# Kernel optimization log

Hardware: AMD Instinct MI355X
Metric: run time of the kernel (lower is better)

Reference implementation:

```python
import jax, jax.numpy as jnp
import numpy as np

INPUT_DIM = 362
HIDDEN = 256
STYLE_NUM = 60
OUTFIT_NUM = 49710
BATCH = 16384


def setup_inputs() -> dict:
    key = jax.random.key(0)
    ks = jax.random.split(key, 12)
    f32 = jnp.float32
    return {
        "i_feature": jax.random.normal(ks[0], (BATCH, INPUT_DIM), f32),
        "j_feature": jax.random.normal(ks[1], (BATCH, INPUT_DIM), f32),
        "k_feature": jax.random.normal(ks[2], (BATCH, INPUT_DIM), f32),
        # top_emb / bottom_emb Linear params (stored transposed: x @ W + b)
        "W_top": jax.random.normal(ks[3], (INPUT_DIM, HIDDEN), f32) * 0.05,
        "b_top": jnp.zeros((HIDDEN,), f32),
        "W_bot": jax.random.normal(ks[4], (INPUT_DIM, HIDDEN), f32) * 0.05,
        "b_bot": jnp.zeros((HIDDEN,), f32),
        # NMF factors (forward relu_'s them in place; we relu on use)
        "P_nmf": jax.random.normal(ks[5], (2 * INPUT_DIM, STYLE_NUM), f32),
        "N_nmf": jax.random.normal(ks[6], (2 * INPUT_DIM, STYLE_NUM), f32),
        "H1_nmf": jax.random.normal(ks[7], (STYLE_NUM, OUTFIT_NUM), f32),
        "H2_nmf": jax.random.normal(ks[8], (STYLE_NUM, OUTFIT_NUM), f32),
        "matirx_pos": jax.random.uniform(ks[9], (2 * INPUT_DIM, OUTFIT_NUM), f32),
        "matirx_neg": jax.random.uniform(ks[10], (2 * INPUT_DIM, OUTFIT_NUM), f32),
    }


def _emb(x, W, b):
    # nn.Sequential(Linear, Sigmoid)
    return jax.nn.sigmoid(x @ W + b)


def _style_score(i_f, j_f, styles, W_top, b_top, W_bot, b_bot):
    # Vectorized version of the per-sample loop:
    # squared-distance argmin codebook lookup + gather + rowwise dot.
    outfit = jnp.concatenate([i_f, j_f], axis=1)  # [B, 2D]
    # mean over feature dim of (x - s)^2; constant 1/(2D) scale does not change argmin
    d2 = (jnp.sum(outfit * outfit, axis=1, keepdims=True)
          - 2.0 * (outfit @ styles)
          + jnp.sum(styles * styles, axis=0, keepdims=True))  # [B, S]
    idx = jnp.argmin(d2, axis=1)                               # [B]
    sel = styles.T[idx]                                        # [B, 2D] gather
    top, bot = sel[:, :INPUT_DIM], sel[:, INPUT_DIM:]
    # diag(matmul) == rowwise dot
    return jnp.sum(_emb(top, W_top, b_top) * _emb(bot, W_bot, b_bot), axis=1)  # [B]


def reference(i_feature, j_feature, k_feature, W_top, b_top, W_bot, b_bot,
              P_nmf, N_nmf, H1_nmf, H2_nmf, matirx_pos, matirx_neg):
    Ti = _emb(i_feature, W_top, b_top)   # [B, H]
    Bj = _emb(j_feature, W_bot, b_bot)   # [B, H]
    Bk = _emb(k_feature, W_bot, b_bot)   # [B, H]
    # torch.diag(matmul(Ti, Bj.T)) == rowwise dot (avoids [B,B] intermediate)
    ij_score = jnp.sum(Ti * Bj, axis=1)  # [B]
    ik_score = jnp.sum(Ti * Bk, axis=1)  # [B]

    # forward does relu_ on .data before use
    P = jnp.maximum(P_nmf, 0.0)
    N = jnp.maximum(N_nmf, 0.0)
    H1 = jnp.maximum(H1_nmf, 0.0)
    H2 = jnp.maximum(H2_nmf, 0.0)

    style_ij = _style_score(i_feature, j_feature, P, W_top, b_top, W_bot, b_bot)
    style_ik = _style_score(i_feature, k_feature, N, W_top, b_top, W_bot, b_bot)

    # -mean(log(sigmoid(d))) computed stably
    loss1 = -jnp.mean(jax.nn.log_sigmoid(ij_score - ik_score))
    loss2 = -jnp.mean(jax.nn.log_sigmoid(style_ij - style_ik))
    loss3 = jnp.mean(jnp.square(matirx_pos - P @ H1)
                     + jnp.square(matirx_neg - N @ H2))
    loss = loss1 + loss2 + 0.1 * loss3

    ij_ik = jnp.stack([ij_score, ik_score], axis=1)  # [B, 2]
    auc = jnp.mean((jnp.argmax(ij_ik, axis=1) == 0).astype(jnp.float32))
    return (loss, loss1, loss2, loss3, auc)
```

## Files before the change

kernel.cpp:

```cpp
#include <hip/hip_runtime.h>
#include <math.h>

#define BATCH 16384
#define IND   362
#define KP    384
#define HID   256
#define STY   60
#define NOUT  49710
#define OUTP  49920
#define D2    724
#define D2P   768

#define NB_HR   3120
#define NB_CW   768
#define NB_CPN  384
#define NB_CF   9216
#define NB_CONV (NB_HR + NB_CW + NB_CPN + NB_CF)

#define NB_SS   120

#define OCH     256
#define N_OC    195
#define DHALF   368
#define NTILES  23
#define NB_M    (2 * 2 * N_OC)

#define NB_EMB  1024
#define NB_SA   512
#define NB_HH   16
#define NB_PPB  2
#define NB_HEAD (NB_HH + NB_PPB)

typedef __bf16 bf16x8 __attribute__((ext_vector_type(8)));
typedef float  floatx4 __attribute__((ext_vector_type(4)));
typedef float  floatx2 __attribute__((ext_vector_type(2)));

__device__ inline floatx4 mfma16(bf16x8 a, bf16x8 b, floatx4 c) {
  return __builtin_amdgcn_mfma_f32_16x16x32_bf16(a, b, c, 0, 0, 0);
}

__device__ inline unsigned short f32_to_bf16(float x) {
  unsigned int u = __float_as_uint(x);
  unsigned int r = (u + 0x7FFFu + ((u >> 16) & 1u)) >> 16;
  return (unsigned short)r;
}

__device__ inline float sigm_fast(float x) { return 1.0f / (1.0f + __expf(-x)); }
__device__ inline float softplusf(float z) { return fmaxf(z, 0.0f) + log1pf(expf(-fabsf(z))); }

__global__ __launch_bounds__(256) void k_conv(
    const float* __restrict__ fi, const float* __restrict__ fj, const float* __restrict__ fk,
    const float* __restrict__ Wt, const float* __restrict__ Wb,
    const float* __restrict__ Pn, const float* __restrict__ Nn,
    const float* __restrict__ H1, const float* __restrict__ H2,
    unsigned short* __restrict__ fbf, unsigned short* __restrict__ wbfT,
    unsigned short* __restrict__ pnbfT, unsigned short* __restrict__ hrows,
    float* __restrict__ Pr) {
  int b = blockIdx.x;
  int t = threadIdx.x;

  if (b < NB_HR) {
    int e = (b * 256 + t) * 8;
    int row = e / OUTP;
    int o = e - row * OUTP;
    int s = row & 63;
    int mm = row >> 6;
    const float* H = mm ? H2 : H1;
    unsigned short* dst = hrows + (size_t)row * OUTP + o;
    unsigned int wv[4];
    if (s < STY && o + 8 <= NOUT) {
      const float* src = H + (size_t)s * NOUT + o;
      #pragma unroll
      for (int ee = 0; ee < 4; ee++) {
        floatx2 v = *(const floatx2*)(src + 2 * ee);
        wv[ee] = (unsigned)f32_to_bf16(fmaxf(v[0], 0.0f)) |
                 ((unsigned)f32_to_bf16(fmaxf(v[1], 0.0f)) << 16);
      }
    } else {
      #pragma unroll
      for (int ee = 0; ee < 4; ee++) {
        float lo = (s < STY && o + 2 * ee     < NOUT) ? fmaxf(H[(size_t)s * NOUT + o + 2 * ee],     0.0f) : 0.0f;
        float hi = (s < STY && o + 2 * ee + 1 < NOUT) ? fmaxf(H[(size_t)s * NOUT + o + 2 * ee + 1], 0.0f) : 0.0f;
        wv[ee] = (unsigned)f32_to_bf16(lo) | ((unsigned)f32_to_bf16(hi) << 16);
      }
    }
    uint4 v; v.x = wv[0]; v.y = wv[1]; v.z = wv[2]; v.w = wv[3];
    *(uint4*)dst = v;
    return;
  }
  b -= NB_HR;

  if (b < NB_CW) {
    int idx = b * 256 + t;
    int k = idx % KP;
    int rem = idx / KP;
    int h = rem % HID;
    int mm = rem / HID;
    const float* W = mm ? Wb : Wt;
    wbfT[idx] = f32_to_bf16(k < IND ? W[(size_t)k * HID + h] : 0.0f);
    return;
  }
  b -= NB_CW;

  if (b < NB_CPN) {
    int u = b * 256 + t;
    int s = u & 63;
    int v = u >> 6;
    int m = (v >= D2P) ? 1 : 0;
    int d = v - m * D2P;
    const float* M = m ? Nn : Pn;
    float x = (d < D2 && s < STY) ? fmaxf(M[(size_t)d * STY + s], 0.0f) : 0.0f;
    unsigned short bb = f32_to_bf16(x);
    int k = (d < IND) ? d : (d < D2 ? d + 22 : (d < 746 ? d - IND : d));
    pnbfT[((size_t)m * 64 + s) * D2P + k] = bb;
    Pr[((size_t)m * D2P + d) * 64 + s] = x;
    return;
  }
  b -= NB_CPN;

  {
    long u = (long)b * 256 + t;
    int g = (int)(u % 48);
    long rf = u / 48;
    int row = (int)(rf % BATCH);
    int f = (int)(rf / BATCH);
    const float* src = (f == 0) ? fi : (f == 1 ? fj : fk);
    int d0 = g * 8;
    const float* sp = src + (size_t)row * IND + d0;
    unsigned int wv[4];
    #pragma unroll
    for (int e = 0; e < 4; e++) {
      int dd = d0 + 2 * e;
      float lo = (dd < IND)     ? sp[2 * e]     : 0.0f;
      float hi = (dd + 1 < IND) ? sp[2 * e + 1] : 0.0f;
      wv[e] = (unsigned)f32_to_bf16(lo) | ((unsigned)f32_to_bf16(hi) << 16);
    }
    uint4 v; v.x = wv[0]; v.y = wv[1]; v.z = wv[2]; v.w = wv[3];
    *(uint4*)(fbf + ((size_t)f * BATCH + row) * KP + d0) = v;
  }
}

__global__ __launch_bounds__(256) void k_style(
    const float* __restrict__ Wt, const float* __restrict__ btop,
    const float* __restrict__ Wb, const float* __restrict__ bbot,
    const float* __restrict__ Pn, const float* __restrict__ Nn,
    float* __restrict__ ss, float* __restrict__ cn) {
  __shared__ float sel[D2];
  __shared__ float shr[4];
  int b = blockIdx.x;
  int t = threadIdx.x;
  int s  = b % STY;
  int mt = b / STY;
  const float* M = mt ? Nn : Pn;
  float cnp = 0.0f;
  for (int d = t; d < D2; d += 256) {
    float v = fmaxf(M[(size_t)d * STY + s], 0.0f);
    sel[d] = v;
    cnp += v * v;
  }
  __syncthreads();
  float at = btop[t], ab = bbot[t];
  for (int d = 0; d < IND; d++) at = fmaf(sel[d],       Wt[(size_t)d * HID + t], at);
  for (int d = 0; d < IND; d++) ab = fmaf(sel[IND + d], Wb[(size_t)d * HID + t], ab);
  float prod = (1.0f / (1.0f + expf(-at))) * (1.0f / (1.0f + expf(-ab)));
  for (int off = 32; off > 0; off >>= 1) prod += __shfl_xor(prod, off);
  if ((t & 63) == 0) shr[t >> 6] = prod;
  __syncthreads();
  if (t == 0) ss[mt * 64 + s] = shr[0] + shr[1] + shr[2] + shr[3];
  __syncthreads();
  for (int off = 32; off > 0; off >>= 1) cnp += __shfl_xor(cnp, off);
  if ((t & 63) == 0) shr[t >> 6] = cnp;
  __syncthreads();
  if (t == 0) cn[mt * 64 + s] = shr[0] + shr[1] + shr[2] + shr[3];
}

__global__ __launch_bounds__(256) void k_m(
    const unsigned short* __restrict__ hrows, const float* __restrict__ Pr,
    const float* __restrict__ mp, const float* __restrict__ mneg,
    float* __restrict__ partial) {
  __shared__ unsigned short Hs[64 * OCH];
  __shared__ float red[4];
  int w = threadIdx.x >> 6, lane = threadIdx.x & 63;
  int m = lane & 15, q = lane >> 4;

  int b = blockIdx.x;
  int oc  = b % N_OC;
  int r   = b / N_OC;
  int dh  = r & 1;
  int mat = r >> 1;
  int o0 = oc * OCH;
  bool full = (o0 + OCH <= NOUT);
  const float* Mbase = mat ? mneg : mp;
  const float* Prb   = Pr + (size_t)mat * D2P * 64;

  char* HsB = (char*)Hs;
  #pragma unroll
  for (int rr = 0; rr < 16; rr++) {
    int R = w * 16 + rr;
    uint2 hv = *(const uint2*)(hrows + ((size_t)mat * 64 + R) * OUTP + o0 + lane * 4);
    *(uint2*)(HsB + R * 512 + ((lane * 8) ^ ((R & 7) << 4))) = hv;
  }
  __syncthreads();

  int xm = (m & 7) << 4;
  float msq = 0.0f, t2 = 0.0f;
  floatx2 mreg[32];
  floatx4 preg[4];

  auto ISSUE_M = [&](int t) {
    int d = dh * DHALF + t * 16 + m;
    bool ok = (d < D2);
    const float* Mr = Mbase + (size_t)d * NOUT + o0 + q * 8;
    if (ok && full) {
      #pragma unroll
      for (int kc = 0; kc < 8; kc++) {
        mreg[kc * 4 + 0] = *(const floatx2*)(Mr + kc * 32);
        mreg[kc * 4 + 1] = *(const floatx2*)(Mr + kc * 32 + 2);
        mreg[kc * 4 + 2] = *(const floatx2*)(Mr + kc * 32 + 4);
        mreg[kc * 4 + 3] = *(const floatx2*)(Mr + kc * 32 + 6);
      }
    } else {
      #pragma unroll
      for (int kc = 0; kc < 8; kc++) {
        #pragma unroll
        for (int e = 0; e < 4; e++) {
          int o = o0 + kc * 32 + q * 8 + 2 * e;
          floatx2 v = {0.f, 0.f};
          if (ok) {
            if (o     < NOUT) v[0] = Mbase[(size_t)d * NOUT + o];
            if (o + 1 < NOUT) v[1] = Mbase[(size_t)d * NOUT + o + 1];
          }
          mreg[kc * 4 + e] = v;
        }
      }
    }
  };
  auto ISSUE_P = [&](int t) {
    int d = dh * DHALF + t * 16 + m;
    const float* Pp = Prb + (size_t)d * 64 + q * 4;
    #pragma unroll
    for (int st = 0; st < 4; st++) preg[st] = *(const floatx4*)(Pp + st * 16);
  };

  int t0 = w;
  if (t0 < NTILES) { ISSUE_M(t0); ISSUE_P(t0); }
  for (int t = t0; t < NTILES; t += 4) {
    bf16x8 bf[8];
    #pragma unroll
    for (int kc = 0; kc < 8; kc++) {
      union { unsigned int u[4]; bf16x8 v; } cv;
      #pragma unroll
      for (int e = 0; e < 4; e++) {
        floatx2 tv = mreg[kc * 4 + e];
        msq = fmaf(tv[0], tv[0], msq);
        msq = fmaf(tv[1], tv[1], msq);
        cv.u[e] = (unsigned)f32_to_bf16(tv[0]) | ((unsigned)f32_to_bf16(tv[1]) << 16);
      }
      bf[kc] = cv.v;
    }
    int tn = t + 4;
    if (tn < NTILES) ISSUE_M(tn);

    floatx4 acc[4];
    #pragma unroll
    for (int st = 0; st < 4; st++) acc[st] = (floatx4){0.f, 0.f, 0.f, 0.f};
    #pragma unroll
    for (int kc = 0; kc < 8; kc++) {
      #pragma unroll
      for (int st = 0; st < 4; st++) {
        bf16x8 hf = *(const bf16x8*)(HsB + (st * 16 + m) * 512 + ((kc * 64 + q * 16) ^ xm));
        acc[st] = mfma16(hf, bf[kc], acc[st]);
      }
    }

    #pragma unroll
    for (int st = 0; st < 4; st++)
      #pragma unroll
      for (int rg = 0; rg < 4; rg++)
        t2 = fmaf(preg[st][rg], acc[st][rg], t2);
    if (tn < NTILES) ISSUE_P(tn);
  }

  float local = msq - 2.0f * t2;
  for (int off = 32; off > 0; off >>= 1) local += __shfl_xor(local, off);
  if (lane == 0) red[w] = local;
  __syncthreads();
  if (threadIdx.x == 0) partial[blockIdx.x] = red[0] + red[1] + red[2] + red[3];
}

__global__ __launch_bounds__(256, 4) void k_emb(
    const unsigned short* __restrict__ fbf, const unsigned short* __restrict__ wbfT,
    const float* __restrict__ btop, const float* __restrict__ bbot,
    float* __restrict__ sIJ, float* __restrict__ sIK) {
  int w = threadIdx.x >> 6, lane = threadIdx.x & 63;
  int m = lane & 15, q = lane >> 4;
  int b = blockIdx.x;
  int r0 = (b & 255) * 64 + w * 16;
  int hb = (b >> 8) * 64;
  const unsigned short* fi = fbf + (size_t)(r0 + m) * KP + q * 8;
  const unsigned short* fj = fi + (size_t)BATCH * KP;
  const unsigned short* fk = fj + (size_t)BATCH * KP;
  floatx4 accI[4], accJ[4], accK[4];
  #pragma unroll
  for (int nt = 0; nt < 4; nt++) {
    accI[nt] = (floatx4){0.f, 0.f, 0.f, 0.f};
    accJ[nt] = (floatx4){0.f, 0.f, 0.f, 0.f};
    accK[nt] = (floatx4){0.f, 0.f, 0.f, 0.f};
  }
  for (int kc = 0; kc < 12; kc++) {
    bf16x8 ai = *(const bf16x8*)(fi + kc * 32);
    bf16x8 aj = *(const bf16x8*)(fj + kc * 32);
    bf16x8 ak = *(const bf16x8*)(fk + kc * 32);
    #pragma unroll
    for (int nt = 0; nt < 4; nt++) {
      int n = hb + nt * 16 + m;
      const unsigned short* wp = wbfT + (size_t)n * KP + kc * 32 + q * 8;
      bf16x8 bt8 = *(const bf16x8*)(wp);
      bf16x8 bb8 = *(const bf16x8*)(wp + (size_t)HID * KP);
      accI[nt] = mfma16(ai, bt8, accI[nt]);
      accJ[nt] = mfma16(aj, bb8, accJ[nt]);
      accK[nt] = mfma16(ak, bb8, accK[nt]);
    }
  }
  float sij[4] = {0.f, 0.f, 0.f, 0.f}, sik[4] = {0.f, 0.f, 0.f, 0.f};
  #pragma unroll
  for (int nt = 0; nt < 4; nt++) {
    int n = hb + nt * 16 + m;
    float vbt = btop[n], vbb = bbot[n];
    #pragma unroll
    for (int reg = 0; reg < 4; reg++) {
      float ti = sigm_fast(accI[nt][reg] + vbt);
      float tj = sigm_fast(accJ[nt][reg] + vbb);
      float tk = sigm_fast(accK[nt][reg] + vbb);
      sij[reg] += ti * tj;
      sik[reg] += ti * tk;
    }
  }
  #pragma unroll
  for (int reg = 0; reg < 4; reg++) {
    for (int off = 1; off < 16; off <<= 1) {
      sij[reg] += __shfl_xor(sij[reg], off);
      sik[reg] += __shfl_xor(sik[reg], off);
    }
  }
  if (m == 0) {
    #pragma unroll
    for (int reg = 0; reg < 4; reg++) {
      int row = r0 + q * 4 + reg;
      atomicAdd(&sIJ[row], sij[reg]);
      atomicAdd(&sIK[row], sik[reg]);
    }
  }
}

__global__ __launch_bounds__(256, 4) void k_sa(
    const unsigned short* __restrict__ fbf, const unsigned short* __restrict__ pnbfT,
    const float* __restrict__ cn, const float* __restrict__ ss,
    float* __restrict__ stIJ, float* __restrict__ stIK) {
  int w = threadIdx.x >> 6, lane = threadIdx.x & 63;
  int m = lane & 15, q = lane >> 4;
  int b = blockIdx.x;
  int mat = w & 1;
  int r0 = b * 32 + (w >> 1) * 16;
  const unsigned short* fA = fbf + (size_t)(r0 + m) * KP + q * 8;
  const unsigned short* fB = fA + (size_t)(1 + mat) * BATCH * KP;
  const unsigned short* Bp = pnbfT + (size_t)mat * 64 * D2P + q * 8;
  floatx4 acc[4];
  #pragma unroll
  for (int nt = 0; nt < 4; nt++) acc[nt] = (floatx4){0.f, 0.f, 0.f, 0.f};
  for (int kc = 0; kc < 24; kc++) {
    bf16x8 a = (kc < 12) ? *(const bf16x8*)(fA + kc * 32)
                         : *(const bf16x8*)(fB + (kc - 12) * 32);
    #pragma unroll
    for (int nt = 0; nt < 4; nt++) {
      bf16x8 bb = *(const bf16x8*)(Bp + (size_t)(nt * 16 + m) * D2P + kc * 32);
      acc[nt] = mfma16(a, bb, acc[nt]);
    }
  }
  const float* cnm = cn + mat * 64;
  float bv[4]; int bi[4];
  #pragma unroll
  for (int reg = 0; reg < 4; reg++) { bv[reg] = __builtin_inff(); bi[reg] = 1 << 30; }
  #pragma unroll
  for (int nt = 0; nt < 4; nt++) {
    int s = nt * 16 + m;
    float c = cnm[s & 63];
    #pragma unroll
    for (int reg = 0; reg < 4; reg++) {
      float d2 = (s < STY) ? (c - 2.0f * acc[nt][reg]) : __builtin_inff();
      if (d2 < bv[reg] || (d2 == bv[reg] && s < bi[reg])) { bv[reg] = d2; bi[reg] = s; }
    }
  }
  for (int off = 1; off < 16; off <<= 1) {
    #pragma unroll
    for (int reg = 0; reg < 4; reg++) {
      float ov = __shfl_xor(bv[reg], off);
      int   oi = __shfl_xor(bi[reg], off);
      if (ov < bv[reg] || (ov == bv[reg] && oi < bi[reg])) { bv[reg] = ov; bi[reg] = oi; }
    }
  }
  if (m == 0) {
    float* dst = mat ? stIK : stIJ;
    const float* ssm = ss + mat * 64;
    #pragma unroll
    for (int reg = 0; reg < 4; reg++) dst[r0 + q * 4 + reg] = ssm[bi[reg]];
  }
}

__global__ __launch_bounds__(256) void k_head(
    const unsigned short* __restrict__ pnbfT, const unsigned short* __restrict__ hrows,
    float* __restrict__ HHb, float* __restrict__ PPb) {
  __shared__ float red[4096];
  int w = threadIdx.x >> 6, lane = threadIdx.x & 63;
  int m = lane & 15, q = lane >> 4;
  int b = blockIdx.x;
  bool isPP = (b >= NB_HH);
  int mat, chunk, nsteps, stride;
  const unsigned short* Rb;
  if (!isPP) { mat = b >> 3; chunk = b & 7; Rb = hrows + (size_t)mat * 64 * OUTP; stride = OUTP; nsteps = 195; }
  else       { mat = b - NB_HH; chunk = 0; Rb = pnbfT + (size_t)mat * 64 * D2P;  stride = D2P;  nsteps = 24;  }
  const unsigned short* Rm = Rb + (size_t)m * stride;

  floatx4 acc[4][4];
  #pragma unroll
  for (int a2 = 0; a2 < 4; a2++)
    #pragma unroll
    for (int b2 = 0; b2 < 4; b2++) acc[a2][b2] = (floatx4){0.f, 0.f, 0.f, 0.f};

  bf16x8 hc[4], hn[4];
  auto LD = [&](int j, bf16x8* hh) {
    int k = (chunk * nsteps + j) * 32 + q * 8;
    #pragma unroll
    for (int st = 0; st < 4; st++)
      hh[st] = *(const bf16x8*)(Rm + (size_t)(st * 16) * stride + k);
  };
  int j = w;
  LD(j, hc);
  for (; j < nsteps; j += 4) {
    if (j + 4 < nsteps) LD(j + 4, hn);
    #pragma unroll
    for (int a2 = 0; a2 < 4; a2++)
      #pragma unroll
      for (int b2 = 0; b2 < 4; b2++)
        acc[a2][b2] = mfma16(hc[a2], hc[b2], acc[a2][b2]);
    #pragma unroll
    for (int st = 0; st < 4; st++) hc[st] = hn[st];
  }
  for (int idx = threadIdx.x; idx < 4096; idx += 256) red[idx] = 0.f;
  __syncthreads();
  #pragma unroll
  for (int a2 = 0; a2 < 4; a2++)
    #pragma unroll
    for (int b2 = 0; b2 < 4; b2++)
      #pragma unroll
      for (int r = 0; r < 4; r++)
        atomicAdd(&red[(a2 * 16 + q * 4 + r) * 64 + b2 * 16 + m], acc[a2][b2][r]);
  __syncthreads();
  float* dst = (isPP ? PPb : HHb) + (size_t)mat * 4096;
  for (int idx = threadIdx.x; idx < 4096; idx += 256) atomicAdd(&dst[idx], red[idx]);
}

__global__ __launch_bounds__(256) void k_final(
    const float* __restrict__ sIJ, const float* __restrict__ sIK,
    const float* __restrict__ stIJ, const float* __restrict__ stIK,
    const float* __restrict__ l3partial,
    const float* __restrict__ HHb, const float* __restrict__ PPb,
    float* __restrict__ out) {
  int t = threadIdx.x;
  float l1 = 0.f, l2 = 0.f, ac = 0.f;
  for (int r = t; r < BATCH; r += 256) {
    float dij = sIJ[r] - sIK[r];
    l1 += softplusf(-dij);
    if (dij >= 0.0f) ac += 1.0f;
    float dst = stIJ[r] - stIK[r];
    l2 += softplusf(-dst);
  }
  double l3 = 0.0;
  for (int p = t; p < NB_M; p += 256) l3 += (double)l3partial[p];
  for (int idx = t; idx < 8192; idx += 256) l3 += (double)HHb[idx] * (double)PPb[idx];
  __shared__ float sh1[4], sh2[4], sh3[4];
  __shared__ double sh4[4];
  for (int off = 32; off > 0; off >>= 1) {
    l1 += __shfl_xor(l1, off);
    l2 += __shfl_xor(l2, off);
    ac += __shfl_xor(ac, off);
    l3 += __shfl_xor(l3, off);
  }
  if ((t & 63) == 0) { sh1[t >> 6] = l1; sh2[t >> 6] = l2; sh3[t >> 6] = ac; sh4[t >> 6] = l3; }
  __syncthreads();
  if (t == 0) {
    double L1 = 0, L2 = 0, AC = 0, L3 = 0;
    for (int i = 0; i < 4; i++) { L1 += sh1[i]; L2 += sh2[i]; AC += sh3[i]; L3 += sh4[i]; }
    L1 /= BATCH; L2 /= BATCH; AC /= BATCH;
    L3 /= ((double)D2 * (double)NOUT);
    out[0] = (float)(L1 + L2 + 0.1 * L3);
    out[1] = (float)L1;
    out[2] = (float)L2;
    out[3] = (float)L3;
    out[4] = (float)AC;
  }
}

extern "C" void kernel_launch(void* const* d_in, const int* in_sizes, int n_in,
                              void* d_out, int out_size, void* d_ws, size_t ws_size,
                              hipStream_t stream) {
  (void)in_sizes; (void)n_in; (void)out_size; (void)ws_size;
  const float* i_f  = (const float*)d_in[0];
  const float* j_f  = (const float*)d_in[1];
  const float* k_f  = (const float*)d_in[2];
  const float* W_t  = (const float*)d_in[3];
  const float* b_t  = (const float*)d_in[4];
  const float* W_b  = (const float*)d_in[5];
  const float* b_b  = (const float*)d_in[6];
  const float* P_n  = (const float*)d_in[7];
  const float* N_n  = (const float*)d_in[8];
  const float* H1   = (const float*)d_in[9];
  const float* H2   = (const float*)d_in[10];
  const float* Mp   = (const float*)d_in[11];
  const float* Mn   = (const float*)d_in[12];
  float* out = (float*)d_out;
  char* ws = (char*)d_ws;

  const size_t OFF_FBF   = 0;
  const size_t OFF_WBFT  = OFF_FBF   + (size_t)3 * BATCH * KP * 2;
  const size_t OFF_PNBFT = OFF_WBFT  + (size_t)2 * HID * KP * 2;
  const size_t OFF_PR    = OFF_PNBFT + (size_t)2 * 64 * D2P * 2;
  const size_t OFF_HROWS = OFF_PR    + (size_t)2 * D2P * 64 * 4;
  const size_t OFF_SIJ   = OFF_HROWS + (size_t)2 * 64 * OUTP * 2;
  const size_t OFF_SIK   = OFF_SIJ   + (size_t)BATCH * 4;
  const size_t OFF_HH    = OFF_SIK   + (size_t)BATCH * 4;
  const size_t OFF_PP    = OFF_HH    + (size_t)2 * 4096 * 4;
  const size_t OFF_STIJ  = OFF_PP    + (size_t)2 * 4096 * 4;
  const size_t OFF_STIK  = OFF_STIJ  + (size_t)BATCH * 4;
  const size_t OFF_SS    = OFF_STIK  + (size_t)BATCH * 4;
  const size_t OFF_CN    = OFF_SS    + 512;
  const size_t OFF_L3P   = OFF_CN    + 512;

  unsigned short* fbf   = (unsigned short*)(ws + OFF_FBF);
  unsigned short* wbfT  = (unsigned short*)(ws + OFF_WBFT);
  unsigned short* pnbfT = (unsigned short*)(ws + OFF_PNBFT);
  float*          Pr    = (float*)(ws + OFF_PR);
  unsigned short* hrows = (unsigned short*)(ws + OFF_HROWS);
  float*  sIJ  = (float*)(ws + OFF_SIJ);
  float*  sIK  = (float*)(ws + OFF_SIK);
  float*  HHb  = (float*)(ws + OFF_HH);
  float*  PPb  = (float*)(ws + OFF_PP);
  float*  stIJ = (float*)(ws + OFF_STIJ);
  float*  stIK = (float*)(ws + OFF_STIK);
  float*  ss   = (float*)(ws + OFF_SS);
  float*  cn   = (float*)(ws + OFF_CN);
  float*  l3p  = (float*)(ws + OFF_L3P);

  hipMemsetAsync(ws + OFF_SIJ, 0, (size_t)BATCH * 4 * 2 + (size_t)4 * 4096 * 4, stream);

  k_conv<<<NB_CONV, 256, 0, stream>>>(i_f, j_f, k_f, W_t, W_b, P_n, N_n, H1, H2,
                                      fbf, wbfT, pnbfT, hrows, Pr);
  k_style<<<NB_SS, 256, 0, stream>>>(W_t, b_t, W_b, b_b, P_n, N_n, ss, cn);
  k_m<<<NB_M, 256, 0, stream>>>(hrows, Pr, Mp, Mn, l3p);
  k_emb<<<NB_EMB, 256, 0, stream>>>(fbf, wbfT, b_t, b_b, sIJ, sIK);
  k_sa<<<NB_SA, 256, 0, stream>>>(fbf, pnbfT, cn, ss, stIJ, stIK);
  k_head<<<NB_HEAD, 256, 0, stream>>>(pnbfT, hrows, HHb, PPb);
  k_final<<<1, 256, 0, stream>>>(sIJ, sIK, stIJ, stIK, l3p, HHb, PPb, out);
}
```

Baseline: 698.6 us.

## Merge seven launches into prep and main kernels with last-block finalize

Replaces the memset plus seven kernel launches with two launches. A prep kernel does the zeroing, style scoring and all conversions. A main kernel dispatches by block index to the M-loss, embedding, style-assignment and head work. The final reduction is done by whichever block finishes last, detected through an atomic counter. This removes launch gaps and tail idle time between small kernels and lets the independent work phases overlap, at the cost of a larger shared-memory footprint for every block type and an atomic-counter handshake.

New measurement: 810.4 us. 16.0% more time.

```diff
diff --git a/kernel.cpp b/kernel.cpp
--- a/kernel.cpp
+++ b/kernel.cpp
@@ -11,25 +11,26 @@
 #define D2    724
 #define D2P   768
 
+#define NB_Z    49
+#define NB_SS   120
 #define NB_HR   3120
 #define NB_CW   768
 #define NB_CPN  384
 #define NB_CF   9216
-#define NB_CONV (NB_HR + NB_CW + NB_CPN + NB_CF)
-
-#define NB_SS   120
+#define NB_PREP (NB_Z + NB_SS + NB_HR + NB_CW + NB_CPN + NB_CF)
+#define ZBYTES  196864
 
 #define OCH     256
 #define N_OC    195
 #define DHALF   368
 #define NTILES  23
-#define NB_M    (2 * 2 * N_OC)
-
+#define NB_MB   (2 * 2 * N_OC)
 #define NB_EMB  1024
 #define NB_SA   512
 #define NB_HH   16
 #define NB_PPB  2
 #define NB_HEAD (NB_HH + NB_PPB)
+#define NB_MAIN (NB_MB + NB_EMB + NB_SA + NB_HEAD)
 
 typedef __bf16 bf16x8 __attribute__((ext_vector_type(8)));
 typedef float  floatx4 __attribute__((ext_vector_type(4)));
@@ -48,16 +49,58 @@
 __device__ inline float sigm_fast(float x) { return 1.0f / (1.0f + __expf(-x)); }
 __device__ inline float softplusf(float z) { return fmaxf(z, 0.0f) + log1pf(expf(-fabsf(z))); }
 
-__global__ __launch_bounds__(256) void k_conv(
+__global__ __launch_bounds__(256) void k_prep(
     const float* __restrict__ fi, const float* __restrict__ fj, const float* __restrict__ fk,
-    const float* __restrict__ Wt, const float* __restrict__ Wb,
+    const float* __restrict__ Wt, const float* __restrict__ btop,
+    const float* __restrict__ Wb, const float* __restrict__ bbot,
     const float* __restrict__ Pn, const float* __restrict__ Nn,
     const float* __restrict__ H1, const float* __restrict__ H2,
     unsigned short* __restrict__ fbf, unsigned short* __restrict__ wbfT,
     unsigned short* __restrict__ pnbfT, unsigned short* __restrict__ hrows,
-    float* __restrict__ Pr) {
+    float* __restrict__ Pr, char* __restrict__ zbase,
+    float* __restrict__ ss, float* __restrict__ cn) {
+  __shared__ float sel[D2];
+  __shared__ float shr[4];
   int b = blockIdx.x;
   int t = threadIdx.x;
+
+  if (b < NB_Z) {
+    size_t idx = ((size_t)b * 256 + t) * 16;
+    if (idx < ZBYTES) {
+      uint4 z; z.x = 0u; z.y = 0u; z.z = 0u; z.w = 0u;
+      *(uint4*)(zbase + idx) = z;
+    }
+    return;
+  }
+  b -= NB_Z;
+
+  if (b < NB_SS) {
+    int s  = b % STY;
+    int mt = b / STY;
+    const float* M = mt ? Nn : Pn;
+    float cnp = 0.0f;
+    for (int d = t; d < D2; d += 256) {
+      float v = fmaxf(M[(size_t)d * STY + s], 0.0f);
+      sel[d] = v;
+      cnp += v * v;
+    }
+    __syncthreads();
+    float at = btop[t], ab = bbot[t];
+    for (int d = 0; d < IND; d++) at = fmaf(sel[d],       Wt[(size_t)d * HID + t], at);
+    for (int d = 0; d < IND; d++) ab = fmaf(sel[IND + d], Wb[(size_t)d * HID + t], ab);
+    float prod = (1.0f / (1.0f + expf(-at))) * (1.0f / (1.0f + expf(-ab)));
+    for (int off = 32; off > 0; off >>= 1) prod += __shfl_xor(prod, off);
+    if ((t & 63) == 0) shr[t >> 6] = prod;
+    __syncthreads();
+    if (t == 0) ss[mt * 64 + s] = shr[0] + shr[1] + shr[2] + shr[3];
+    __syncthreads();
+    for (int off = 32; off > 0; off >>= 1) cnp += __shfl_xor(cnp, off);
+    if ((t & 63) == 0) shr[t >> 6] = cnp;
+    __syncthreads();
+    if (t == 0) cn[mt * 64 + s] = shr[0] + shr[1] + shr[2] + shr[3];
+    return;
+  }
+  b -= NB_SS;
 
   if (b < NB_HR) {
     int e = (b * 256 + t) * 8;
@@ -119,11 +162,11 @@
   b -= NB_CPN;
 
   {
-    long u = (long)b * 256 + t;
-    int g = (int)(u % 48);
-    long rf = u / 48;
-    int row = (int)(rf % BATCH);
-    int f = (int)(rf / BATCH);
+    int u = b * 256 + t;
+    int g = u % 48;
+    int rf = u / 48;
+    int row = rf % BATCH;
+    int f = rf / BATCH;
     const float* src = (f == 0) ? fi : (f == 1 ? fj : fk);
     int d0 = g * 8;
     const float* sp = src + (size_t)row * IND + d0;
@@ -140,364 +183,325 @@
   }
 }
 
-__global__ __launch_bounds__(256) void k_style(
-    const float* __restrict__ Wt, const float* __restrict__ btop,
-    const float* __restrict__ Wb, const float* __restrict__ bbot,
-    const float* __restrict__ Pn, const float* __restrict__ Nn,
-    float* __restrict__ ss, float* __restrict__ cn) {
-  __shared__ float sel[D2];
-  __shared__ float shr[4];
-  int b = blockIdx.x;
-  int t = threadIdx.x;
-  int s  = b % STY;
-  int mt = b / STY;
-  const float* M = mt ? Nn : Pn;
-  float cnp = 0.0f;
-  for (int d = t; d < D2; d += 256) {
-    float v = fmaxf(M[(size_t)d * STY + s], 0.0f);
-    sel[d] = v;
-    cnp += v * v;
-  }
-  __syncthreads();
-  float at = btop[t], ab = bbot[t];
-  for (int d = 0; d < IND; d++) at = fmaf(sel[d],       Wt[(size_t)d * HID + t], at);
-  for (int d = 0; d < IND; d++) ab = fmaf(sel[IND + d], Wb[(size_t)d * HID + t], ab);
-  float prod = (1.0f / (1.0f + expf(-at))) * (1.0f / (1.0f + expf(-ab)));
-  for (int off = 32; off > 0; off >>= 1) prod += __shfl_xor(prod, off);
-  if ((t & 63) == 0) shr[t >> 6] = prod;
-  __syncthreads();
-  if (t == 0) ss[mt * 64 + s] = shr[0] + shr[1] + shr[2] + shr[3];
-  __syncthreads();
-  for (int off = 32; off > 0; off >>= 1) cnp += __shfl_xor(cnp, off);
-  if ((t & 63) == 0) shr[t >> 6] = cnp;
-  __syncthreads();
-  if (t == 0) cn[mt * 64 + s] = shr[0] + shr[1] + shr[2] + shr[3];
-}
-
-__global__ __launch_bounds__(256) void k_m(
-    const unsigned short* __restrict__ hrows, const float* __restrict__ Pr,
+__global__ __launch_bounds__(256) void k_main(
+    const unsigned short* __restrict__ fbf, const unsigned short* __restrict__ wbfT,
+    const unsigned short* __restrict__ pnbfT, const unsigned short* __restrict__ hrows,
+    const float* __restrict__ Pr,
+    const float* __restrict__ btop, const float* __restrict__ bbot,
+    const float* __restrict__ cn, const float* __restrict__ ss,
     const float* __restrict__ mp, const float* __restrict__ mneg,
-    float* __restrict__ partial) {
-  __shared__ unsigned short Hs[64 * OCH];
-  __shared__ float red[4];
-  int w = threadIdx.x >> 6, lane = threadIdx.x & 63;
-  int m = lane & 15, q = lane >> 4;
-
-  int b = blockIdx.x;
-  int oc  = b % N_OC;
-  int r   = b / N_OC;
-  int dh  = r & 1;
-  int mat = r >> 1;
-  int o0 = oc * OCH;
-  bool full = (o0 + OCH <= NOUT);
-  const float* Mbase = mat ? mneg : mp;
-  const float* Prb   = Pr + (size_t)mat * D2P * 64;
-
-  char* HsB = (char*)Hs;
-  #pragma unroll
-  for (int rr = 0; rr < 16; rr++) {
-    int R = w * 16 + rr;
-    uint2 hv = *(const uint2*)(hrows + ((size_t)mat * 64 + R) * OUTP + o0 + lane * 4);
-    *(uint2*)(HsB + R * 512 + ((lane * 8) ^ ((R & 7) << 4))) = hv;
-  }
-  __syncthreads();
-
-  int xm = (m & 7) << 4;
-  float msq = 0.0f, t2 = 0.0f;
-  floatx2 mreg[32];
-  floatx4 preg[4];
-
-  auto ISSUE_M = [&](int t) {
-    int d = dh * DHALF + t * 16 + m;
-    bool ok = (d < D2);
-    const float* Mr = Mbase + (size_t)d * NOUT + o0 + q * 8;
-    if (ok && full) {
-      #pragma unroll
-      for (int kc = 0; kc < 8; kc++) {
-        mreg[kc * 4 + 0] = *(const floatx2*)(Mr + kc * 32);
-        mreg[kc * 4 + 1] = *(const floatx2*)(Mr + kc * 32 + 2);
-        mreg[kc * 4 + 2] = *(const floatx2*)(Mr + kc * 32 + 4);
-        mreg[kc * 4 + 3] = *(const floatx2*)(Mr + kc * 32 + 6);
-      }
-    } else {
-      #pragma unroll
-      for (int kc = 0; kc < 8; kc++) {
-        #pragma unroll
-        for (int e = 0; e < 4; e++) {
-          int o = o0 + kc * 32 + q * 8 + 2 * e;
-          floatx2 v = {0.f, 0.f};
-          if (ok) {
-            if (o     < NOUT) v[0] = Mbase[(size_t)d * NOUT + o];
-            if (o + 1 < NOUT) v[1] = Mbase[(size_t)d * NOUT + o + 1];
-          }
-          mreg[kc * 4 + e] = v;
-        }
-      }
-    }
-  };
-  auto ISSUE_P = [&](int t) {
-    int d = dh * DHALF + t * 16 + m;
-    const float* Pp = Prb + (size_t)d * 64 + q * 4;
-    #pragma unroll
-    for (int st = 0; st < 4; st++) preg[st] = *(const floatx4*)(Pp + st * 16);
-  };
-
-  int t0 = w;
-  if (t0 < NTILES) { ISSUE_M(t0); ISSUE_P(t0); }
-  for (int t = t0; t < NTILES; t += 4) {
-    bf16x8 bf[8];
-    #pragma unroll
-    for (int kc = 0; kc < 8; kc++) {
-      union { unsigned int u[4]; bf16x8 v; } cv;
-      #pragma unroll
-      for (int e = 0; e < 4; e++) {
-        floatx2 tv = mreg[kc * 4 + e];
-        msq = fmaf(tv[0], tv[0], msq);
-        msq = fmaf(tv[1], tv[1], msq);
-        cv.u[e] = (unsigned)f32_to_bf16(tv[0]) | ((unsigned)f32_to_bf16(tv[1]) << 16);
-      }
-      bf[kc] = cv.v;
-    }
-    int tn = t + 4;
-    if (tn < NTILES) ISSUE_M(tn);
-
-    floatx4 acc[4];
-    #pragma unroll
-    for (int st = 0; st < 4; st++) acc[st] = (floatx4){0.f, 0.f, 0.f, 0.f};
-    #pragma unroll
-    for (int kc = 0; kc < 8; kc++) {
-      #pragma unroll
-      for (int st = 0; st < 4; st++) {
-        bf16x8 hf = *(const bf16x8*)(HsB + (st * 16 + m) * 512 + ((kc * 64 + q * 16) ^ xm));
-        acc[st] = mfma16(hf, bf[kc], acc[st]);
-      }
-    }
-
-    #pragma unroll
-    for (int st = 0; st < 4; st++)
-      #pragma unroll
-      for (int rg = 0; rg < 4; rg++)
-        t2 = fmaf(preg[st][rg], acc[st][rg], t2);
-    if (tn < NTILES) ISSUE_P(tn);
-  }
-
-  float local = msq - 2.0f * t2;
-  for (int off = 32; off > 0; off >>= 1) local += __shfl_xor(local, off);
-  if (lane == 0) red[w] = local;
-  __syncthreads();
-  if (threadIdx.x == 0) partial[blockIdx.x] = red[0] + red[1] + red[2] + red[3];
-}
-
-__global__ __launch_bounds__(256, 4) void k_emb(
-    const unsigned short* __restrict__ fbf, const unsigned short* __restrict__ wbfT,
-    const float* __restrict__ btop, const float* __restrict__ bbot,
-    float* __restrict__ sIJ, float* __restrict__ sIK) {
+    float* __restrict__ sIJ, float* __restrict__ sIK,
+    float* __restrict__ stIJ, float* __restrict__ stIK,
+    float* __restrict__ HHb, float* __restrict__ PPb,
+    float* __restrict__ partial, unsigned int* __restrict__ cnt,
+    float* __restrict__ out) {
+  __shared__ __align__(16) char smem[32896];
   int w = threadIdx.x >> 6, lane = threadIdx.x & 63;
   int m = lane & 15, q = lane >> 4;
   int b = blockIdx.x;
-  int r0 = (b & 255) * 64 + w * 16;
-  int hb = (b >> 8) * 64;
-  const unsigned short* fi = fbf + (size_t)(r0 + m) * KP + q * 8;
-  const unsigned short* fj = fi + (size_t)BATCH * KP;
-  const unsigned short* fk = fj + (size_t)BATCH * KP;
-  floatx4 accI[4], accJ[4], accK[4];
-  #pragma unroll
-  for (int nt = 0; nt < 4; nt++) {
-    accI[nt] = (floatx4){0.f, 0.f, 0.f, 0.f};
-    accJ[nt] = (floatx4){0.f, 0.f, 0.f, 0.f};
-    accK[nt] = (floatx4){0.f, 0.f, 0.f, 0.f};
-  }
-  for (int kc = 0; kc < 12; kc++) {
-    bf16x8 ai = *(const bf16x8*)(fi + kc * 32);
-    bf16x8 aj = *(const bf16x8*)(fj + kc * 32);
-    bf16x8 ak = *(const bf16x8*)(fk + kc * 32);
+
+  if (b < NB_MB) {
+    char* HsB = smem;
+    float* shp = (float*)(smem + 32768);
+    int oc  = b % N_OC;
+    int r   = b / N_OC;
+    int dh  = r & 1;
+    int mat = r >> 1;
+    int o0 = oc * OCH;
+    bool full = (o0 + OCH <= NOUT);
+    const float* Mbase = mat ? mneg : mp;
+    const float* Prb   = Pr + (size_t)mat * D2P * 64;
+
+    #pragma unroll
+    for (int rr = 0; rr < 16; rr++) {
+      int R = w * 16 + rr;
+      uint2 hv = *(const uint2*)(hrows + ((size_t)mat * 64 + R) * OUTP + o0 + lane * 4);
+      *(uint2*)(HsB + R * 512 + ((lane * 8) ^ ((R & 7) << 4))) = hv;
+    }
+    __syncthreads();
+
+    int xm = (m & 7) << 4;
+    float msq = 0.0f, t2 = 0.0f;
+    floatx2 mreg[32];
+    floatx4 preg[4];
+
+    auto ISSUE_M = [&](int t) {
+      int d = dh * DHALF + t * 16 + m;
+      bool ok = (d < D2);
+      const float* Mr = Mbase + (size_t)d * NOUT + o0 + q * 8;
+      if (ok && full) {
+        #pragma unroll
+        for (int kc = 0; kc < 8; kc++) {
+          mreg[kc * 4 + 0] = *(const floatx2*)(Mr + kc * 32);
+          mreg[kc * 4 + 1] = *(const floatx2*)(Mr + kc * 32 + 2);
+          mreg[kc * 4 + 2] = *(const floatx2*)(Mr + kc * 32 + 4);
+          mreg[kc * 4 + 3] = *(const floatx2*)(Mr + kc * 32 + 6);
+        }
+      } else {
+        #pragma unroll
+        for (int kc = 0; kc < 8; kc++) {
+          #pragma unroll
+          for (int e = 0; e < 4; e++) {
+            int o = o0 + kc * 32 + q * 8 + 2 * e;
+            floatx2 v = {0.f, 0.f};
+            if (ok) {
+              if (o     < NOUT) v[0] = Mbase[(size_t)d * NOUT + o];
+              if (o + 1 < NOUT) v[1] = Mbase[(size_t)d * NOUT + o + 1];
+            }
+            mreg[kc * 4 + e] = v;
+          }
+        }
+      }
+    };
+    auto ISSUE_P = [&](int t) {
+      int d = dh * DHALF + t * 16 + m;
+      const float* Pp = Prb + (size_t)d * 64 + q * 4;
+      #pragma unroll
+      for (int st = 0; st < 4; st++) preg[st] = *(const floatx4*)(Pp + st * 16);
+    };
+
+    int t0 = w;
+    if (t0 < NTILES) { ISSUE_M(t0); ISSUE_P(t0); }
+    for (int t = t0; t < NTILES; t += 4) {
+      bf16x8 bf[8];
+      #pragma unroll
+      for (int kc = 0; kc < 8; kc++) {
+        union { unsigned int u[4]; bf16x8 v; } cv;
+        #pragma unroll
+        for (int e = 0; e < 4; e++) {
+          floatx2 tv = mreg[kc * 4 + e];
+          msq = fmaf(tv[0], tv[0], msq);
+          msq = fmaf(tv[1], tv[1], msq);
+          cv.u[e] = (unsigned)f32_to_bf16(tv[0]) | ((unsigned)f32_to_bf16(tv[1]) << 16);
+        }
+        bf[kc] = cv.v;
+      }
+      int tn = t + 4;
+      if (tn < NTILES) ISSUE_M(tn);
+
+      floatx4 acc[4];
+      #pragma unroll
+      for (int st = 0; st < 4; st++) acc[st] = (floatx4){0.f, 0.f, 0.f, 0.f};
+      #pragma unroll
+      for (int kc = 0; kc < 8; kc++) {
+        #pragma unroll
+        for (int st = 0; st < 4; st++) {
+          bf16x8 hf = *(const bf16x8*)(HsB + (st * 16 + m) * 512 + ((kc * 64 + q * 16) ^ xm));
+          acc[st] = mfma16(hf, bf[kc], acc[st]);
+        }
+      }
+      #pragma unroll
+      for (int st = 0; st < 4; st++)
+        #pragma unroll
+        for (int rg = 0; rg < 4; rg++)
+          t2 = fmaf(preg[st][rg], acc[st][rg], t2);
+      if (tn < NTILES) ISSUE_P(tn);
+    }
+
+    float local = msq - 2.0f * t2;
+    for (int off = 32; off > 0; off >>= 1) local += __shfl_xor(local, off);
+    if (lane == 0) shp[w] = local;
+    __syncthreads();
+    if (threadIdx.x == 0) partial[b] = shp[0] + shp[1] + shp[2] + shp[3];
+  } else if (b < NB_MB + NB_EMB) {
+    int bb2 = b - NB_MB;
+    int r0 = (bb2 & 255) * 64 + w * 16;
+    int hb = (bb2 >> 8) * 64;
+    const unsigned short* fi = fbf + (size_t)(r0 + m) * KP + q * 8;
+    const unsigned short* fj = fi + (size_t)BATCH * KP;
+    const unsigned short* fk = fj + (size_t)BATCH * KP;
+    floatx4 accI[4], accJ[4], accK[4];
+    #pragma unroll
+    for (int nt = 0; nt < 4; nt++) {
+      accI[nt] = (floatx4){0.f, 0.f, 0.f, 0.f};
+      accJ[nt] = (floatx4){0.f, 0.f, 0.f, 0.f};
+      accK[nt] = (floatx4){0.f, 0.f, 0.f, 0.f};
+    }
+    for (int kc = 0; kc < 12; kc++) {
+      bf16x8 ai = *(const bf16x8*)(fi + kc * 32);
+      bf16x8 aj = *(const bf16x8*)(fj + kc * 32);
+      bf16x8 ak = *(const bf16x8*)(fk + kc * 32);
+      #pragma unroll
+      for (int nt = 0; nt < 4; nt++) {
+        int n = hb + nt * 16 + m;
+        const unsigned short* wp = wbfT + (size_t)n * KP + kc * 32 + q * 8;
+        bf16x8 bt8 = *(const bf16x8*)(wp);
+        bf16x8 bb8 = *(const bf16x8*)(wp + (size_t)HID * KP);
+        accI[nt] = mfma16(ai, bt8, accI[nt]);
+        accJ[nt] = mfma16(aj, bb8, accJ[nt]);
+        accK[nt] = mfma16(ak, bb8, accK[nt]);
+      }
+    }
+    float sij[4] = {0.f, 0.f, 0.f, 0.f}, sik[4] = {0.f, 0.f, 0.f, 0.f};
     #pragma unroll
     for (int nt = 0; nt < 4; nt++) {
       int n = hb + nt * 16 + m;
-      const unsigned short* wp = wbfT + (size_t)n * KP + kc * 32 + q * 8;
-      bf16x8 bt8 = *(const bf16x8*)(wp);
-      bf16x8 bb8 = *(const bf16x8*)(wp + (size_t)HID * KP);
-      accI[nt] = mfma16(ai, bt8, accI[nt]);
-      accJ[nt] = mfma16(aj, bb8, accJ[nt]);
-      accK[nt] = mfma16(ak, bb8, accK[nt]);
-    }
-  }
-  float sij[4] = {0.f, 0.f, 0.f, 0.f}, sik[4] = {0.f, 0.f, 0.f, 0.f};
-  #pragma unroll
-  for (int nt = 0; nt < 4; nt++) {
-    int n = hb + nt * 16 + m;
-    float vbt = btop[n], vbb = bbot[n];
+      float vbt = btop[n], vbb = bbot[n];
+      #pragma unroll
+      for (int reg = 0; reg < 4; reg++) {
+        float ti = sigm_fast(accI[nt][reg] + vbt);
+        float tj = sigm_fast(accJ[nt][reg] + vbb);
+        float tk = sigm_fast(accK[nt][reg] + vbb);
+        sij[reg] += ti * tj;
+        sik[reg] += ti * tk;
+      }
+    }
     #pragma unroll
     for (int reg = 0; reg < 4; reg++) {
-      float ti = sigm_fast(accI[nt][reg] + vbt);
-      float tj = sigm_fast(accJ[nt][reg] + vbb);
-      float tk = sigm_fast(accK[nt][reg] + vbb);
-      sij[reg] += ti * tj;
-      sik[reg] += ti * tk;
-    }
-  }
-  #pragma unroll
-  for (int reg = 0; reg < 4; reg++) {
+      for (int off = 1; off < 16; off <<= 1) {
+        sij[reg] += __shfl_xor(sij[reg], off);
+        sik[reg] += __shfl_xor(sik[reg], off);
+      }
+    }
+    if (m == 0) {
+      #pragma unroll
+      for (int reg = 0; reg < 4; reg++) {
+        int row = r0 + q * 4 + reg;
+        atomicAdd(&sIJ[row], sij[reg]);
+        atomicAdd(&sIK[row], sik[reg]);
+      }
+    }
+  } else if (b < NB_MB + NB_EMB + NB_SA) {
+    int bb2 = b - NB_MB - NB_EMB;
+    int mat = w & 1;
+    int r0 = bb2 * 32 + (w >> 1) * 16;
+    const unsigned short* fA = fbf + (size_t)(r0 + m) * KP + q * 8;
+    const unsigned short* fB = fA + (size_t)(1 + mat) * BATCH * KP;
+    const unsigned short* Bp = pnbfT + (size_t)mat * 64 * D2P + q * 8;
+    floatx4 acc[4];
+    #pragma unroll
+    for (int nt = 0; nt < 4; nt++) acc[nt] = (floatx4){0.f, 0.f, 0.f, 0.f};
+    for (int kc = 0; kc < 24; kc++) {
+      bf16x8 a = (kc < 12) ? *(const bf16x8*)(fA + kc * 32)
+                           : *(const bf16x8*)(fB + (kc - 12) * 32);
+      #pragma unroll
+      for (int nt = 0; nt < 4; nt++) {
+        bf16x8 bb8 = *(const bf16x8*)(Bp + (size_t)(nt * 16 + m) * D2P + kc * 32);
+        acc[nt] = mfma16(a, bb8, acc[nt]);
+      }
+    }
+    const float* cnm = cn + mat * 64;
+    float bv[4]; int bi[4];
+    #pragma unroll
+    for (int reg = 0; reg < 4; reg++) { bv[reg] = __builtin_inff(); bi[reg] = 1 << 30; }
+    #pragma unroll
+    for (int nt = 0; nt < 4; nt++) {
+      int s = nt * 16 + m;
+      float c = cnm[s & 63];
+      #pragma unroll
+      for (int reg = 0; reg < 4; reg++) {
+        float d2 = (s < STY) ? (c - 2.0f * acc[nt][reg]) : __builtin_inff();
+        if (d2 < bv[reg] || (d2 == bv[reg] && s < bi[reg])) { bv[reg] = d2; bi[reg] = s; }
+      }
+    }
     for (int off = 1; off < 16; off <<= 1) {
-      sij[reg] += __shfl_xor(sij[reg], off);
-      sik[reg] += __shfl_xor(sik[reg], off);
-    }
-  }
-  if (m == 0) {
-    #pragma unroll
-    for (int reg = 0; reg < 4; reg++) {
-      int row = r0 + q * 4 + reg;
-      atomicAdd(&sIJ[row], sij[reg]);
-      atomicAdd(&sIK[row], sik[reg]);
-    }
-  }
-}
-
-__global__ __launch_bounds__(256, 4) void k_sa(
-    const unsigned short* __restrict__ fbf, const unsigned short* __restrict__ pnbfT,
-    const float* __restrict__ cn, const float* __restrict__ ss,
-    float* __restrict__ stIJ, float* __restrict__ stIK) {
-  int w = threadIdx.x >> 6, lane = threadIdx.x & 63;
-  int m = lane & 15, q = lane >> 4;
-  int b = blockIdx.x;
-  int mat = w & 1;
-  int r0 = b * 32 + (w >> 1) * 16;
-  const unsigned short* fA = fbf + (size_t)(r0 + m) * KP + q * 8;
-  const unsigned short* fB = fA + (size_t)(1 + mat) * BATCH * KP;
-  const unsigned short* Bp = pnbfT + (size_t)mat * 64 * D2P + q * 8;
-  floatx4 acc[4];
-  #pragma unroll
-  for (int nt = 0; nt < 4; nt++) acc[nt] = (floatx4){0.f, 0.f, 0.f, 0.f};
-  for (int kc = 0; kc < 24; kc++) {
-    bf16x8 a = (kc < 12) ? *(const bf16x8*)(fA + kc * 32)
-                         : *(const bf16x8*)(fB + (kc - 12) * 32);
-    #pragma unroll
-    for (int nt = 0; nt < 4; nt++) {
-      bf16x8 bb = *(const bf16x8*)(Bp + (size_t)(nt * 16 + m) * D2P + kc * 32);
-      acc[nt] = mfma16(a, bb, acc[nt]);
-    }
-  }
-  const float* cnm = cn + mat * 64;
-  float bv[4]; int bi[4];
-  #pragma unroll
-  for (int reg = 0; reg < 4; reg++) { bv[reg] = __builtin_inff(); bi[reg] = 1 << 30; }
-  #pragma unroll
-  for (int nt = 0; nt < 4; nt++) {
-    int s = nt * 16 + m;
-    float c = cnm[s & 63];
-    #pragma unroll
-    for (int reg = 0; reg < 4; reg++) {
-      float d2 = (s < STY) ? (c - 2.0f * acc[nt][reg]) : __builtin_inff();
-      if (d2 < bv[reg] || (d2 == bv[reg] && s < bi[reg])) { bv[reg] = d2; bi[reg] = s; }
-    }
-  }
-  for (int off = 1; off < 16; off <<= 1) {
-    #pragma unroll
-    for (int reg = 0; reg < 4; reg++) {
-      float ov = __shfl_xor(bv[reg], off);
-      int   oi = __shfl_xor(bi[reg], off);
-      if (ov < bv[reg] || (ov == bv[reg] && oi < bi[reg])) { bv[reg] = ov; bi[reg] = oi; }
-    }
-  }
-  if (m == 0) {
-    float* dst = mat ? stIK : stIJ;
-    const float* ssm = ss + mat * 64;
-    #pragma unroll
-    for (int reg = 0; reg < 4; reg++) dst[r0 + q * 4 + reg] = ssm[bi[reg]];
-  }
-}
-
-__global__ __launch_bounds__(256) void k_head(
-    const unsigned short* __restrict__ pnbfT, const unsigned short* __restrict__ hrows,
-    float* __restrict__ HHb, float* __restrict__ PPb) {
-  __shared__ float red[4096];
-  int w = threadIdx.x >> 6, lane = threadIdx.x & 63;
-  int m = lane & 15, q = lane >> 4;
-  int b = blockIdx.x;
-  bool isPP = (b >= NB_HH);
-  int mat, chunk, nsteps, stride;
-  const unsigned short* Rb;
-  if (!isPP) { mat = b >> 3; chunk = b & 7; Rb = hrows + (size_t)mat * 64 * OUTP; stride = OUTP; nsteps = 195; }
-  else       { mat = b - NB_HH; chunk = 0; Rb = pnbfT + (size_t)mat * 64 * D2P;  stride = D2P;  nsteps = 24;  }
-  const unsigned short* Rm = Rb + (size_t)m * stride;
-
-  floatx4 acc[4][4];
-  #pragma unroll
-  for (int a2 = 0; a2 < 4; a2++)
-    #pragma unroll
-    for (int b2 = 0; b2 < 4; b2++) acc[a2][b2] = (floatx4){0.f, 0.f, 0.f, 0.f};
-
-  bf16x8 hc[4], hn[4];
-  auto LD = [&](int j, bf16x8* hh) {
-    int k = (chunk * nsteps + j) * 32 + q * 8;
-    #pragma unroll
-    for (int st = 0; st < 4; st++)
-      hh[st] = *(const bf16x8*)(Rm + (size_t)(st * 16) * stride + k);
-  };
-  int j = w;
-  LD(j, hc);
-  for (; j < nsteps; j += 4) {
-    if (j + 4 < nsteps) LD(j + 4, hn);
+      #pragma unroll
+      for (int reg = 0; reg < 4; reg++) {
+        float ov = __shfl_xor(bv[reg], off);
+        int   oi = __shfl_xor(bi[reg], off);
+        if (ov < bv[reg] || (ov == bv[reg] && oi < bi[reg])) { bv[reg] = ov; bi[reg] = oi; }
+      }
+    }
+    if (m == 0) {
+      float* dst = mat ? stIK : stIJ;
+      const float* ssm = ss + mat * 64;
+      #pragma unroll
+      for (int reg = 0; reg < 4; reg++) dst[r0 + q * 4 + reg] = ssm[bi[reg]];
+    }
+  } else {
+    int bb2 = b - NB_MB - NB_EMB - NB_SA;
+    float* red = (float*)smem;
+    bool isPP = (bb2 >= NB_HH);
+    int mat, chunk, nsteps, stride;
+    const unsigned short* Rb;
+    if (!isPP) { mat = bb2 >> 3; chunk = bb2 & 7; Rb = hrows + (size_t)mat * 64 * OUTP; stride = OUTP; nsteps = 195; }
+    else       { mat = bb2 - NB_HH; chunk = 0; Rb = pnbfT + (size_t)mat * 64 * D2P;  stride = D2P;  nsteps = 24;  }
+    const unsigned short* Rm = Rb + (size_t)m * stride;
+
+    floatx4 acc[4][4];
     #pragma unroll
     for (int a2 = 0; a2 < 4; a2++)
       #pragma unroll
+      for (int b2 = 0; b2 < 4; b2++) acc[a2][b2] = (floatx4){0.f, 0.f, 0.f, 0.f};
+
+    bf16x8 hc[4], hn[4];
+    auto LD = [&](int j, bf16x8* hh) {
+      int k = (chunk * nsteps + j) * 32 + q * 8;
+      #pragma unroll
+      for (int st = 0; st < 4; st++)
+        hh[st] = *(const bf16x8*)(Rm + (size_t)(st * 16) * stride + k);
+    };
+    int j = w;
+    LD(j, hc);
+    for (; j < nsteps; j += 4) {
+      if (j + 4 < nsteps) LD(j + 4, hn);
+      #pragma unroll
+      for (int a2 = 0; a2 < 4; a2++)
+        #pragma unroll
+        for (int b2 = 0; b2 < 4; b2++)
+          acc[a2][b2] = mfma16(hc[a2], hc[b2], acc[a2][b2]);
+      #pragma unroll
+      for (int st = 0; st < 4; st++) hc[st] = hn[st];
+    }
+    for (int idx = threadIdx.x; idx < 4096; idx += 256) red[idx] = 0.f;
+    __syncthreads();
+    #pragma unroll
+    for (int a2 = 0; a2 < 4; a2++)
+      #pragma unroll
       for (int b2 = 0; b2 < 4; b2++)
-        acc[a2][b2] = mfma16(hc[a2], hc[b2], acc[a2][b2]);
-    #pragma unroll
-    for (int st = 0; st < 4; st++) hc[st] = hn[st];
-  }
-  for (int idx = threadIdx.x; idx < 4096; idx += 256) red[idx] = 0.f;
+        #pragma unroll
+        for (int r = 0; r < 4; r++)
+          atomicAdd(&red[(a2 * 16 + q * 4 + r) * 64 + b2 * 16 + m], acc[a2][b2][r]);
+    __syncthreads();
+    float* dst = (isPP ? PPb : HHb) + (size_t)mat * 4096;
+    for (int idx = threadIdx.x; idx < 4096; idx += 256) atomicAdd(&dst[idx], red[idx]);
+  }
+
   __syncthreads();
-  #pragma unroll
-  for (int a2 = 0; a2 < 4; a2++)
-    #pragma unroll
-    for (int b2 = 0; b2 < 4; b2++)
-      #pragma unroll
-      for (int r = 0; r < 4; r++)
-        atomicAdd(&red[(a2 * 16 + q * 4 + r) * 64 + b2 * 16 + m], acc[a2][b2][r]);
+  __threadfence();
+  unsigned int* flag = (unsigned int*)(smem + 32768 + 96);
+  if (threadIdx.x == 0) {
+    unsigned int old = atomicAdd(cnt, 1u);
+    *flag = (old == (unsigned int)(NB_MAIN - 1)) ? 1u : 0u;
+  }
   __syncthreads();
-  float* dst = (isPP ? PPb : HHb) + (size_t)mat * 4096;
-  for (int idx = threadIdx.x; idx < 4096; idx += 256) atomicAdd(&dst[idx], red[idx]);
-}
-
-__global__ __launch_bounds__(256) void k_final(
-    const float* __restrict__ sIJ, const float* __restrict__ sIK,
-    const float* __restrict__ stIJ, const float* __restrict__ stIK,
-    const float* __restrict__ l3partial,
-    const float* __restrict__ HHb, const float* __restrict__ PPb,
-    float* __restrict__ out) {
-  int t = threadIdx.x;
-  float l1 = 0.f, l2 = 0.f, ac = 0.f;
-  for (int r = t; r < BATCH; r += 256) {
-    float dij = sIJ[r] - sIK[r];
-    l1 += softplusf(-dij);
-    if (dij >= 0.0f) ac += 1.0f;
-    float dst = stIJ[r] - stIK[r];
-    l2 += softplusf(-dst);
-  }
-  double l3 = 0.0;
-  for (int p = t; p < NB_M; p += 256) l3 += (double)l3partial[p];
-  for (int idx = t; idx < 8192; idx += 256) l3 += (double)HHb[idx] * (double)PPb[idx];
-  __shared__ float sh1[4], sh2[4], sh3[4];
-  __shared__ double sh4[4];
-  for (int off = 32; off > 0; off >>= 1) {
-    l1 += __shfl_xor(l1, off);
-    l2 += __shfl_xor(l2, off);
-    ac += __shfl_xor(ac, off);
-    l3 += __shfl_xor(l3, off);
-  }
-  if ((t & 63) == 0) { sh1[t >> 6] = l1; sh2[t >> 6] = l2; sh3[t >> 6] = ac; sh4[t >> 6] = l3; }
-  __syncthreads();
-  if (t == 0) {
-    double L1 = 0, L2 = 0, AC = 0, L3 = 0;
-    for (int i = 0; i < 4; i++) { L1 += sh1[i]; L2 += sh2[i]; AC += sh3[i]; L3 += sh4[i]; }
-    L1 /= BATCH; L2 /= BATCH; AC /= BATCH;
-    L3 /= ((double)D2 * (double)NOUT);
-    out[0] = (float)(L1 + L2 + 0.1 * L3);
-    out[1] = (float)L1;
-    out[2] = (float)L2;
-    out[3] = (float)L3;
-    out[4] = (float)AC;
+  if (*flag) {
+    __threadfence();
+    int t = threadIdx.x;
+    float l1 = 0.f, l2 = 0.f, ac = 0.f;
+    for (int r = t; r < BATCH; r += 256) {
+      float dij = sIJ[r] - sIK[r];
+      l1 += softplusf(-dij);
+      if (dij >= 0.0f) ac += 1.0f;
+      float dst = stIJ[r] - stIK[r];
+      l2 += softplusf(-dst);
+    }
+    double l3 = 0.0;
+    for (int p = t; p < NB_MB; p += 256) l3 += (double)partial[p];
+    for (int idx = t; idx < 8192; idx += 256) l3 += (double)HHb[idx] * (double)PPb[idx];
+    float* sh1 = (float*)(smem + 32768);
+    float* sh2 = sh1 + 4;
+    float* sh3 = sh2 + 4;
+    double* sh4 = (double*)(smem + 32768 + 48);
+    for (int off = 32; off > 0; off >>= 1) {
+      l1 += __shfl_xor(l1, off);
+      l2 += __shfl_xor(l2, off);
+      ac += __shfl_xor(ac, off);
+      l3 += __shfl_xor(l3, off);
+    }
+    if ((t & 63) == 0) { sh1[t >> 6] = l1; sh2[t >> 6] = l2; sh3[t >> 6] = ac; sh4[t >> 6] = l3; }
+    __syncthreads();
+    if (t == 0) {
+      double L1 = 0, L2 = 0, AC = 0, L3 = 0;
+      for (int i = 0; i < 4; i++) { L1 += sh1[i]; L2 += sh2[i]; AC += sh3[i]; L3 += sh4[i]; }
+      L1 /= BATCH; L2 /= BATCH; AC /= BATCH;
+      L3 /= ((double)D2 * (double)NOUT);
+      out[0] = (float)(L1 + L2 + 0.1 * L3);
+      out[1] = (float)L1;
+      out[2] = (float)L2;
+      out[3] = (float)L3;
+      out[4] = (float)AC;
+    }
   }
 }
 
@@ -530,7 +534,8 @@
   const size_t OFF_SIK   = OFF_SIJ   + (size_t)BATCH * 4;
   const size_t OFF_HH    = OFF_SIK   + (size_t)BATCH * 4;
   const size_t OFF_PP    = OFF_HH    + (size_t)2 * 4096 * 4;
-  const size_t OFF_STIJ  = OFF_PP    + (size_t)2 * 4096 * 4;
+  const size_t OFF_CNT   = OFF_PP    + (size_t)2 * 4096 * 4;
+  const size_t OFF_STIJ  = OFF_CNT   + 256;
   const size_t OFF_STIK  = OFF_STIJ  + (size_t)BATCH * 4;
   const size_t OFF_SS    = OFF_STIK  + (size_t)BATCH * 4;
   const size_t OFF_CN    = OFF_SS    + 512;
@@ -545,20 +550,19 @@
   float*  sIK  = (float*)(ws + OFF_SIK);
   float*  HHb  = (float*)(ws + OFF_HH);
   float*  PPb  = (float*)(ws + OFF_PP);
+  unsigned int* cnt = (unsigned int*)(ws + OFF_CNT);
   float*  stIJ = (float*)(ws + OFF_STIJ);
   float*  stIK = (float*)(ws + OFF_STIK);
   float*  ss   = (float*)(ws + OFF_SS);
   float*  cn   = (float*)(ws + OFF_CN);
   float*  l3p  = (float*)(ws + OFF_L3P);
 
-  hipMemsetAsync(ws + OFF_SIJ, 0, (size_t)BATCH * 4 * 2 + (size_t)4 * 4096 * 4, stream);
-
-  k_conv<<<NB_CONV, 256, 0, stream>>>(i_f, j_f, k_f, W_t, W_b, P_n, N_n, H1, H2,
-                                      fbf, wbfT, pnbfT, hrows, Pr);
-  k_style<<<NB_SS, 256, 0, stream>>>(W_t, b_t, W_b, b_b, P_n, N_n, ss, cn);
-  k_m<<<NB_M, 256, 0, stream>>>(hrows, Pr, Mp, Mn, l3p);
-  k_emb<<<NB_EMB, 256, 0, stream>>>(fbf, wbfT, b_t, b_b, sIJ, sIK);
-  k_sa<<<NB_SA, 256, 0, stream>>>(fbf, pnbfT, cn, ss, stIJ, stIK);
-  k_head<<<NB_HEAD, 256, 0, stream>>>(pnbfT, hrows, HHb, PPb);
-  k_final<<<1, 256, 0, stream>>>(sIJ, sIK, stIJ, stIK, l3p, HHb, PPb, out);
+  k_prep<<<NB_PREP, 256, 0, stream>>>(i_f, j_f, k_f, W_t, b_t, W_b, b_b,
+                                      P_n, N_n, H1, H2,
+                                      fbf, wbfT, pnbfT, hrows, Pr,
+                                      ws + OFF_SIJ, ss, cn);
+  k_main<<<NB_MAIN, 256, 0, stream>>>(fbf, wbfT, pnbfT, hrows, Pr,
+                                      b_t, b_b, cn, ss, Mp, Mn,
+                                      sIJ, sIK, stIJ, stIK, HHb, PPb, l3p,
+                                      cnt, out);
 }
```
